# Kernel tuning notes

Hardware: AMD Instinct MI355X
Metric: run time of the kernel (lower is better)

The kernel has to match this reference:

```python
import math
import jax, jax.numpy as jnp
import numpy as np

# Module config (init_kwargs)
GRID = (11, 16, 24)          # (T, H, W) latent grid, T odd so T-1 == 2*(T//2)
POOL = 128                   # pool_size / block size
SPARSITY = 0.9
TXT_LEN = 384                # txt_len, txt_first=False
HEADS, HDIM = 8, 128
FFL = GRID[1] * GRID[2]      # first_frame_len = H*W = 384
SEQ = GRID[0] * FFL + TXT_LEN  # 4608 tokens, 36 blocks of 128


def _rearr(t):
    # rearrange_with_remaining, h%8==0 and w%8==0 path.
    # t: [b, (f h w), n, d] with f = T-1 frames (first frame excluded)
    b, s, n, d = t.shape
    T, H, W = GRID
    fn, hn, wn = T // 2, H // 8, W // 8
    x = t.transpose(0, 2, 1, 3).reshape(b * n, fn, 2, hn, 8, wn, 8, d)
    # 'b (fn fb)(hn hb)(wn wb) d -> b (fn hn wn fb hb wb) d'
    x = x.transpose(0, 1, 3, 5, 2, 4, 6, 7).reshape(b * n, s, d)
    return x.reshape(b, n, s, d).transpose(0, 2, 1, 3)


def _inv_rearr(t):
    b, s, n, d = t.shape
    T, H, W = GRID
    fn, hn, wn = T // 2, H // 8, W // 8
    x = t.transpose(0, 2, 1, 3).reshape(b * n, fn, hn, wn, 2, 8, 8, d)
    x = x.transpose(0, 1, 4, 2, 5, 3, 6, 7).reshape(b * n, s, d)
    return x.reshape(b, n, s, d).transpose(0, 2, 1, 3)


def _avgpool(t):
    # seq divisible by POOL -> mean over each block (tail branch unused)
    b, s, n, d = t.shape
    return t.reshape(b, s // POOL, POOL, n, d).mean(axis=2)


def _forward(q, k, v):
    b, s, n, d = q.shape
    scale = jnp.asarray(d, q.dtype) ** -0.5
    # do_tensor_rearrange_pooling on concatenated qkv (txt_first=False)
    qkv = jnp.concatenate([q, k, v], axis=0)
    f_part = qkv[:, :FFL]
    i_part = qkv[:, FFL:s - TXT_LEN]
    t_part = qkv[:, s - TXT_LEN:]
    qkv2 = jnp.concatenate([_rearr(i_part), f_part, t_part], axis=1)
    pool = _avgpool(qkv2)
    q2, k2, v2 = jnp.split(qkv2, 3, axis=0)
    qp, kp, _ = jnp.split(pool, 3, axis=0)
    # pooled block scores + softmax
    ps = jax.nn.softmax(jnp.einsum('blnd,bsnd->bnls', qp, kp) * scale, axis=-1)
    nb = s // POOL
    keep = math.ceil(nb * (1.0 - SPARSITY))
    thr = jax.lax.top_k(ps, keep)[0][..., -1:]
    mask = ps >= thr                              # [B, n, nb, nb] bool
    prot = (FFL + TXT_LEN + POOL - 1) // POOL
    mask = mask.at[:, :, -prot:, :].set(True)
    mask = mask.at[:, :, :, -prot:].set(True)
    bm = mask[0]                                  # [n, nb, nb] per-head block mask (batch 0, as kernel uses)
    tok = jnp.repeat(jnp.repeat(bm, POOL, axis=1), POOL, axis=2)  # [n, S, S]
    # block-sparse attention == masked dense attention over selected kv blocks
    scores = jnp.einsum('bqnd,bknd->bnqk', q2, k2) * scale
    scores = jnp.where(tok[None], scores, jnp.asarray(-1e30, scores.dtype))
    p = jax.nn.softmax(scores, axis=-1)
    x = jnp.einsum('bnqk,bknd->bqnd', p, v2)
    # do_tensor_inv_rearrange (txt_first=False: concat(f, i, t))
    si = s - TXT_LEN - FFL
    xi = _inv_rearr(x[:, :si])
    xf = x[:, si:si + FFL]
    xt = x[:, si + FFL:]
    return jnp.concatenate([xf, xi, xt], axis=1)


def setup_inputs() -> dict:
    key = jax.random.key(0)
    kq, kk, kv = jax.random.split(key, 3)
    q = jax.random.normal(kq, (1, SEQ, HEADS, HDIM), dtype=jnp.float32)
    k = jax.random.normal(kk, (1, SEQ, HEADS, HDIM), dtype=jnp.float32)
    v = jax.random.normal(kv, (1, SEQ, HEADS, HDIM), dtype=jnp.float32)
    t_b_idx = jnp.arange(2, dtype=jnp.int64 if jax.config.jax_enable_x64 else jnp.int32)
    return {'q': q, 'k': k, 'v': v, 't_b_idx': t_b_idx}


def reference(q, k, v, t_b_idx):
    # t_idx = t_b_idx[0] = 0, skip_timesteps = 0 -> sparse branch (static)
    return _forward(q, k, v)
```

## Files before the change

### kernel.cpp

```cpp
#include <hip/hip_runtime.h>


typedef __attribute__((ext_vector_type(8))) _Float16 half8;
typedef __attribute__((ext_vector_type(4))) _Float16 half4;
typedef __attribute__((ext_vector_type(4))) float float4v;

#define KROW 136
#define VROW 72
#define PROW 72

__device__ __forceinline__ int orig_pos(int j) {
    if (j >= 3840) return (j < 4224) ? (j - 3840) : j;
    int blk = j >> 7;
    int r   = j & 127;
    int f   = blk / 6;
    int rem = blk - f * 6;
    int b2  = rem / 3;
    int e   = rem - b2 * 3;
    int a   = r >> 6;
    int c   = (r >> 3) & 7;
    int g   = r & 7;
    return 384 + (f * 2 + a) * 384 + (b2 * 8 + c) * 24 + e * 8 + g;
}

__device__ __forceinline__ void cp16(const void* g, void* l) {
    __builtin_amdgcn_global_load_lds((const __attribute__((address_space(1))) void*)g,
                                     (__attribute__((address_space(3))) void*)l, 16, 0, 0);
}

__global__ __launch_bounds__(256) void prep_kernel(const float* __restrict__ q,
                                                   const float* __restrict__ k,
                                                   const float* __restrict__ v,
                                                   short* __restrict__ Kc,
                                                   unsigned* __restrict__ Vt32,
                                                   float* __restrict__ qp,
                                                   float* __restrict__ kp) {
    __shared__ short Vs[64 * KROW];
    __shared__ float Rs[8 * 128];
    int bx  = blockIdx.x;
    int tid = threadIdx.x;
    int sub = bx & 1;
    int kb  = (bx >> 1) % 36;
    int h   = bx / 72;

    {
        int lr = tid >> 3;
        int ld = (tid & 7) << 2;
#pragma unroll
        for (int pass = 0; pass < 2; ++pass) {
            int lt  = pass * 32 + lr;
            int tok = sub * 64 + lt;
            int op  = orig_pos(kb * 128 + tok);
            const float* kr = k + ((size_t)op * 8 + h) * 128;
            const float* vr = v + ((size_t)op * 8 + h) * 128;
            short* ko = Kc + ((size_t)(h * 36 + kb) * 128 + tok) * KROW;
#pragma unroll
            for (int j = 0; j < 4; ++j) {
                int d = ld + j * 32;
                float4v xk = *reinterpret_cast<const float4v*>(kr + d);
                float4v xv = *reinterpret_cast<const float4v*>(vr + d);
                half4 hk, hv;
#pragma unroll
                for (int i = 0; i < 4; ++i) { hk[i] = (_Float16)xk[i]; hv[i] = (_Float16)xv[i]; }
                *reinterpret_cast<half4*>(ko + d) = hk;
                *reinterpret_cast<half4*>(&Vs[lt * KROW + d]) = hv;
            }
        }
    }

    {
        const float* arr = sub ? q : k;
        int dq = (tid & 31) << 2;
        int g  = tid >> 5;
        float4v acc = {0.f, 0.f, 0.f, 0.f};
        for (int t = g; t < 128; t += 8) {
            int op = orig_pos(kb * 128 + t);
            float4v x = *reinterpret_cast<const float4v*>(arr + ((size_t)op * 8 + h) * 128 + dq);
            acc[0] += x[0]; acc[1] += x[1]; acc[2] += x[2]; acc[3] += x[3];
        }
#pragma unroll
        for (int i = 0; i < 4; ++i) Rs[g * 128 + dq + i] = acc[i];
    }
    __syncthreads();

    {
        const unsigned short* Vsu = (const unsigned short*)Vs;
        unsigned* vo = Vt32 + (size_t)((h * 36 + kb) * 2 + sub) * 128 * (VROW / 2);
#pragma unroll
        for (int it = 0; it < 16; ++it) {
            int i   = it * 256 + tid;
            int tw  = i & 31;
            int dim = i >> 5;
            unsigned lo = Vsu[(2 * tw) * KROW + dim];
            unsigned hi = Vsu[(2 * tw + 1) * KROW + dim];
            vo[dim * (VROW / 2) + tw] = (hi << 16) | lo;
        }
    }

    if (tid < 128) {
        float s = 0.f;
#pragma unroll
        for (int g = 0; g < 8; ++g) s += Rs[g * 128 + tid];
        float* outp = sub ? qp : kp;
        outp[(h * 36 + kb) * 128 + tid] = s * (1.f / 128.f);
    }
}

__global__ __launch_bounds__(256, 3) void flash_kernel(const float* __restrict__ q,
                                                       const short* __restrict__ Kc,
                                                       const short* __restrict__ Vt,
                                                       const float* __restrict__ qp,
                                                       const float* __restrict__ kp,
                                                       float* __restrict__ out,
                                                       float* __restrict__ pO,
                                                       float* __restrict__ pL) {
    __shared__ __align__(16) short Ks[64 * KROW];
    __shared__ __align__(16) short Vsh[128 * VROW];
    __shared__ __align__(16) short Ph[4 * 16 * PROW];
    __shared__ int Ls[40];

    int t = blockIdx.x;
    int h, qb, half, nkb = 0, kbase = 0, pidx = -1;
    if (t < 288) {
        h = t & 7;
        int rest = t >> 3;
        int qbh = rest / 6, r2 = rest % 6;
        half = r2 / 3;
        int chunk = r2 % 3;
        qb = 30 + qbh; nkb = 12; kbase = chunk * 12; pidx = t;
    } else {
        int t2 = t - 288;
        h = t2 & 7;
        int rest = t2 >> 3;
        qb = rest >> 1; half = rest & 1;
    }

    int tid = threadIdx.x, wave = tid >> 6, lane = tid & 63;
    int m16 = lane & 15, quad = lane >> 4;

    int qrow_frag = qb * 128 + half * 64 + wave * 16 + m16;
    const float* qrp = q + ((size_t)orig_pos(qrow_frag) * 8 + h) * 128;
    half8 aq[4];
#pragma unroll
    for (int kc = 0; kc < 4; ++kc) {
        float4v x0 = *reinterpret_cast<const float4v*>(qrp + kc * 32 + quad * 8);
        float4v x1 = *reinterpret_cast<const float4v*>(qrp + kc * 32 + quad * 8 + 4);
#pragma unroll
        for (int j = 0; j < 4; ++j) { aq[kc][j] = (_Float16)x0[j]; aq[kc][4 + j] = (_Float16)x1[j]; }
    }

    if (pidx < 0 && wave == 0) {
        float s = -1e30f;
        if (lane < 36) {
            const float4v* qv = (const float4v*)(qp + (h * 36 + qb) * 128);
            const float4v* kv = (const float4v*)(kp + (h * 36 + lane) * 128);
            float acc = 0.f;
            for (int i = 0; i < 32; ++i) {
                float4v a = qv[i], b = kv[i];
                acc += a[0] * b[0] + a[1] * b[1] + a[2] * b[2] + a[3] * b[3];
            }
            s = acc;
        }
        float tmp = s;
        float thr = 0.f;
        for (int i = 0; i < 4; ++i) {
            float mx = tmp;
            for (int off = 1; off < 64; off <<= 1) mx = fmaxf(mx, __shfl_xor(mx, off));
            thr = mx;
            unsigned long long bal = __ballot(tmp == mx);
            int low = __ffsll(bal) - 1;
            if (lane == low) tmp = -3e38f;
        }
        bool keep = (lane < 36) && ((s >= thr) || (lane >= 30));
        unsigned long long mk = __ballot(keep);
        if (lane == 0) Ls[0] = __popcll(mk);
        if (keep) {
            int pos = __popcll(mk & ((1ull << lane) - 1ull));
            Ls[1 + pos] = lane;
        }
    }
    __syncthreads();
    if (pidx < 0) nkb = Ls[0];

    float l_r[4], o[8][4];
#pragma unroll
    for (int r = 0; r < 4; ++r) l_r[r] = 0.f;
#pragma unroll
    for (int dt = 0; dt < 8; ++dt)
#pragma unroll
        for (int r = 0; r < 4; ++r) o[dt][r] = 0.f;

    constexpr float kScale = 0.08838834764831845f * 1.4426950408889634f;
    short* Phw = Ph + wave * (16 * PROW);

    int ntile = nkb * 2;
    for (int it = 0; it < ntile; ++it) {
        int kb  = (pidx >= 0) ? (kbase + (it >> 1)) : Ls[1 + (it >> 1)];
        int sub = it & 1;
        const char* gK = (const char*)(Kc + ((size_t)((h * 36 + kb) * 128) + sub * 64) * KROW);
        const char* gV = (const char*)(Vt + (size_t)((h * 36 + kb) * 2 + sub) * 128 * VROW);

        __syncthreads();
        {
            char* lK = (char*)Ks;
            char* lV = (char*)Vsh;
            int off = lane * 16;
            for (int c = wave; c < 35; c += 4) {
                if (c < 17) cp16(gK + c * 1024 + off, lK + c * 1024 + off);
                else        cp16(gV + (c - 17) * 1024 + off, lV + (c - 17) * 1024 + off);
            }
        }
        __syncthreads();

        float4v sacc[4];
#pragma unroll
        for (int nt = 0; nt < 4; ++nt) { sacc[nt][0] = 0.f; sacc[nt][1] = 0.f; sacc[nt][2] = 0.f; sacc[nt][3] = 0.f; }
#pragma unroll
        for (int nt = 0; nt < 4; ++nt)
#pragma unroll
            for (int kc = 0; kc < 4; ++kc) {
                half8 bk = *reinterpret_cast<const half8*>(&Ks[(nt * 16 + m16) * KROW + kc * 32 + quad * 8]);
                sacc[nt] = __builtin_amdgcn_mfma_f32_16x16x32_f16(aq[kc], bk, sacc[nt], 0, 0, 0);
            }

#pragma unroll
        for (int r = 0; r < 4; ++r) {
            float p0 = exp2f(sacc[0][r] * kScale);
            float p1 = exp2f(sacc[1][r] * kScale);
            float p2 = exp2f(sacc[2][r] * kScale);
            float p3 = exp2f(sacc[3][r] * kScale);
            sacc[0][r] = p0; sacc[1][r] = p1; sacc[2][r] = p2; sacc[3][r] = p3;
            l_r[r] += (p0 + p1) + (p2 + p3);
        }

#pragma unroll
        for (int nt = 0; nt < 4; ++nt)
#pragma unroll
            for (int r = 0; r < 4; ++r) {
                union { _Float16 hf; short s; } cv;
                cv.hf = (_Float16)sacc[nt][r];
                Phw[(quad * 4 + r) * PROW + nt * 16 + m16] = cv.s;
            }
        half8 ap0 = *reinterpret_cast<const half8*>(&Phw[m16 * PROW + quad * 8]);
        half8 ap1 = *reinterpret_cast<const half8*>(&Phw[m16 * PROW + 32 + quad * 8]);

#pragma unroll
        for (int dt = 0; dt < 8; ++dt) {
            float4v oc;
            oc[0] = o[dt][0]; oc[1] = o[dt][1]; oc[2] = o[dt][2]; oc[3] = o[dt][3];
            half8 bv0 = *reinterpret_cast<const half8*>(&Vsh[(dt * 16 + m16) * VROW + quad * 8]);
            half8 bv1 = *reinterpret_cast<const half8*>(&Vsh[(dt * 16 + m16) * VROW + 32 + quad * 8]);
            oc = __builtin_amdgcn_mfma_f32_16x16x32_f16(ap0, bv0, oc, 0, 0, 0);
            oc = __builtin_amdgcn_mfma_f32_16x16x32_f16(ap1, bv1, oc, 0, 0, 0);
            o[dt][0] = oc[0]; o[dt][1] = oc[1]; o[dt][2] = oc[2]; o[dt][3] = oc[3];
        }
    }

#pragma unroll
    for (int r = 0; r < 4; ++r)
        for (int sh = 1; sh < 16; sh <<= 1) l_r[r] += __shfl_xor(l_r[r], sh);

    if (pidx >= 0) {
        float* po = pO + (size_t)pidx * 8192;
#pragma unroll
        for (int r = 0; r < 4; ++r) {
            int row = wave * 16 + quad * 4 + r;
#pragma unroll
            for (int dt = 0; dt < 8; ++dt)
                po[row * 128 + dt * 16 + m16] = o[dt][r];
            if (m16 == 0) pL[pidx * 64 + row] = l_r[r];
        }
    } else {
#pragma unroll
        for (int r = 0; r < 4; ++r) {
            int qrow = qb * 128 + half * 64 + wave * 16 + quad * 4 + r;
            size_t base = ((size_t)orig_pos(qrow) * 8 + h) * 128;
            float inv = 1.f / l_r[r];
#pragma unroll
            for (int dt = 0; dt < 8; ++dt)
                out[base + dt * 16 + m16] = o[dt][r] * inv;
        }
    }
}

__global__ void combine_kernel(const float* __restrict__ pO, const float* __restrict__ pL,
                               float* __restrict__ out) {
    int g = blockIdx.x;
    int h    = g / 12;
    int rem  = g % 12;
    int qbh  = rem >> 1;
    int half = rem & 1;
    int qb   = 30 + qbh;
    int base_t = (qbh * 6 + half * 3) * 8 + h;

    int tid = threadIdx.x;
    int d   = tid & 127;
    int r0  = tid >> 7;
    for (int itr = 0; itr < 32; ++itr) {
        int row = r0 + itr * 2;
        float l = pL[(base_t + 0) * 64 + row] + pL[(base_t + 8) * 64 + row] + pL[(base_t + 16) * 64 + row];
        float acc = pO[(size_t)(base_t + 0) * 8192 + row * 128 + d]
                  + pO[(size_t)(base_t + 8) * 8192 + row * 128 + d]
                  + pO[(size_t)(base_t + 16) * 8192 + row * 128 + d];
        int qrow = qb * 128 + half * 64 + row;
        out[((size_t)orig_pos(qrow) * 8 + h) * 128 + d] = acc / l;
    }
}

extern "C" void kernel_launch(void* const* d_in, const int* in_sizes, int n_in,
                              void* d_out, int out_size, void* d_ws, size_t ws_size,
                              hipStream_t stream) {
    const float* q = (const float*)d_in[0];
    const float* k = (const float*)d_in[1];
    const float* v = (const float*)d_in[2];
    float* out = (float*)d_out;

    char* w = (char*)d_ws;
    short* Kc  = (short*)(w);
    short* Vt  = (short*)(w + 10027008);
    float* qp  = (float*)(w + 20643840);
    float* kp  = (float*)(w + 20791296);
    float* pL  = (float*)(w + 20938752);
    float* pO  = (float*)(w + 21012480);

    prep_kernel<<<dim3(576), dim3(256), 0, stream>>>(q, k, v, Kc, (unsigned*)Vt, qp, kp);
    flash_kernel<<<dim3(768), dim3(256), 0, stream>>>(q, Kc, Vt, qp, kp, out, pO, pL);
    combine_kernel<<<dim3(96), dim3(256), 0, stream>>>(pO, pL, out);
}
```

Measured before the change: 191.2 us.

## Use 32x32 MFMA with 128-row query blocks and fuse split-K combine via atomics

Moves the flash kernel from 16x16x32 to 32x32x16 MFMA so each block handles 128 query rows (32 per wave) instead of 64. The heavy protected rows are split four ways over 9 key blocks each rather than three ways over 12. The separate combine kernel is replaced by a last-arriver reduction driven by an atomic counter, and the softmax scale is folded into Q at load time. This cuts the grid to 432 blocks, removes one kernel launch and halves K/V reloads per query row. In exchange it uses more registers (occupancy hint lowered to 2), adds a memset, and needs threadfence and atomic synchronisation.

Result: slower. 217.6 us (+13.8%).

```diff
diff --git a/kernel.cpp b/kernel.cpp
--- a/kernel.cpp
+++ b/kernel.cpp
@@ -4,6 +4,7 @@
 typedef __attribute__((ext_vector_type(8))) _Float16 half8;
 typedef __attribute__((ext_vector_type(4))) _Float16 half4;
 typedef __attribute__((ext_vector_type(4))) float float4v;
+typedef __attribute__((ext_vector_type(16))) float float16v;
 
 #define KROW 136
 #define VROW 72
@@ -26,6 +27,12 @@
 __device__ __forceinline__ void cp16(const void* g, void* l) {
     __builtin_amdgcn_global_load_lds((const __attribute__((address_space(1))) void*)g,
                                      (__attribute__((address_space(3))) void*)l, 16, 0, 0);
+}
+
+__device__ __forceinline__ short h16(float x) {
+    union { _Float16 hf; short s; } cv;
+    cv.hf = (_Float16)x;
+    return cv.s;
 }
 
 __global__ __launch_bounds__(256) void prep_kernel(const float* __restrict__ q,
@@ -106,50 +113,53 @@
     }
 }
 
-__global__ __launch_bounds__(256, 3) void flash_kernel(const float* __restrict__ q,
+__global__ __launch_bounds__(256, 2) void flash_kernel(const float* __restrict__ q,
                                                        const short* __restrict__ Kc,
                                                        const short* __restrict__ Vt,
                                                        const float* __restrict__ qp,
                                                        const float* __restrict__ kp,
                                                        float* __restrict__ out,
                                                        float* __restrict__ pO,
-                                                       float* __restrict__ pL) {
+                                                       float* __restrict__ pL,
+                                                       int* __restrict__ cnt) {
     __shared__ __align__(16) short Ks[64 * KROW];
     __shared__ __align__(16) short Vsh[128 * VROW];
-    __shared__ __align__(16) short Ph[4 * 16 * PROW];
+    __shared__ __align__(16) short Ph[4 * 32 * PROW];
     __shared__ int Ls[40];
 
     int t = blockIdx.x;
-    int h, qb, half, nkb = 0, kbase = 0, pidx = -1;
-    if (t < 288) {
+    int h, qb, qbh = 0, nkb = 0, kbase = 0, task = -1, grp = -1;
+    bool heavy = (t < 192);
+    if (heavy) {
         h = t & 7;
         int rest = t >> 3;
-        int qbh = rest / 6, r2 = rest % 6;
-        half = r2 / 3;
-        int chunk = r2 % 3;
-        qb = 30 + qbh; nkb = 12; kbase = chunk * 12; pidx = t;
+        qbh = rest >> 2;
+        int chunk = rest & 3;
+        qb = 30 + qbh; nkb = 9; kbase = chunk * 9;
+        task = t; grp = qbh * 8 + h;
     } else {
-        int t2 = t - 288;
-        h = t2 & 7;
-        int rest = t2 >> 3;
-        qb = rest >> 1; half = rest & 1;
+        int t2 = t - 192;
+        h = t2 & 7; qb = t2 >> 3;
     }
 
     int tid = threadIdx.x, wave = tid >> 6, lane = tid & 63;
-    int m16 = lane & 15, quad = lane >> 4;
-
-    int qrow_frag = qb * 128 + half * 64 + wave * 16 + m16;
-    const float* qrp = q + ((size_t)orig_pos(qrow_frag) * 8 + h) * 128;
-    half8 aq[4];
-#pragma unroll
-    for (int kc = 0; kc < 4; ++kc) {
-        float4v x0 = *reinterpret_cast<const float4v*>(qrp + kc * 32 + quad * 8);
-        float4v x1 = *reinterpret_cast<const float4v*>(qrp + kc * 32 + quad * 8 + 4);
-#pragma unroll
-        for (int j = 0; j < 4; ++j) { aq[kc][j] = (_Float16)x0[j]; aq[kc][4 + j] = (_Float16)x1[j]; }
-    }
-
-    if (pidx < 0 && wave == 0) {
+    int m32 = lane & 31, half = lane >> 5;
+
+    constexpr float kScale = 0.08838834764831845f * 1.4426950408889634f;
+    const float* qrp = q + ((size_t)orig_pos(qb * 128 + wave * 32 + m32) * 8 + h) * 128 + half * 8;
+    half8 aq[8];
+#pragma unroll
+    for (int kc = 0; kc < 8; ++kc) {
+        float4v x0 = *reinterpret_cast<const float4v*>(qrp + kc * 16);
+        float4v x1 = *reinterpret_cast<const float4v*>(qrp + kc * 16 + 4);
+#pragma unroll
+        for (int j = 0; j < 4; ++j) {
+            aq[kc][j]     = (_Float16)(x0[j] * kScale);
+            aq[kc][4 + j] = (_Float16)(x1[j] * kScale);
+        }
+    }
+
+    if (!heavy && wave == 0) {
         float s = -1e30f;
         if (lane < 36) {
             const float4v* qv = (const float4v*)(qp + (h * 36 + qb) * 128);
@@ -180,22 +190,22 @@
         }
     }
     __syncthreads();
-    if (pidx < 0) nkb = Ls[0];
-
-    float l_r[4], o[8][4];
-#pragma unroll
-    for (int r = 0; r < 4; ++r) l_r[r] = 0.f;
-#pragma unroll
-    for (int dt = 0; dt < 8; ++dt)
-#pragma unroll
-        for (int r = 0; r < 4; ++r) o[dt][r] = 0.f;
-
-    constexpr float kScale = 0.08838834764831845f * 1.4426950408889634f;
-    short* Phw = Ph + wave * (16 * PROW);
+    if (!heavy) nkb = Ls[0];
+
+    float16v oc[4];
+    float l_r[16];
+#pragma unroll
+    for (int dn = 0; dn < 4; ++dn)
+#pragma unroll
+        for (int i = 0; i < 16; ++i) oc[dn][i] = 0.f;
+#pragma unroll
+    for (int r = 0; r < 16; ++r) l_r[r] = 0.f;
+
+    short* Phw = Ph + wave * (32 * PROW);
 
     int ntile = nkb * 2;
     for (int it = 0; it < ntile; ++it) {
-        int kb  = (pidx >= 0) ? (kbase + (it >> 1)) : Ls[1 + (it >> 1)];
+        int kb  = heavy ? (kbase + (it >> 1)) : Ls[1 + (it >> 1)];
         int sub = it & 1;
         const char* gK = (const char*)(Kc + ((size_t)((h * 36 + kb) * 128) + sub * 64) * KROW);
         const char* gV = (const char*)(Vt + (size_t)((h * 36 + kb) * 2 + sub) * 128 * VROW);
@@ -212,98 +222,97 @@
         }
         __syncthreads();
 
-        float4v sacc[4];
-#pragma unroll
-        for (int nt = 0; nt < 4; ++nt) { sacc[nt][0] = 0.f; sacc[nt][1] = 0.f; sacc[nt][2] = 0.f; sacc[nt][3] = 0.f; }
-#pragma unroll
-        for (int nt = 0; nt < 4; ++nt)
-#pragma unroll
-            for (int kc = 0; kc < 4; ++kc) {
-                half8 bk = *reinterpret_cast<const half8*>(&Ks[(nt * 16 + m16) * KROW + kc * 32 + quad * 8]);
-                sacc[nt] = __builtin_amdgcn_mfma_f32_16x16x32_f16(aq[kc], bk, sacc[nt], 0, 0, 0);
-            }
-
-#pragma unroll
-        for (int r = 0; r < 4; ++r) {
-            float p0 = exp2f(sacc[0][r] * kScale);
-            float p1 = exp2f(sacc[1][r] * kScale);
-            float p2 = exp2f(sacc[2][r] * kScale);
-            float p3 = exp2f(sacc[3][r] * kScale);
-            sacc[0][r] = p0; sacc[1][r] = p1; sacc[2][r] = p2; sacc[3][r] = p3;
-            l_r[r] += (p0 + p1) + (p2 + p3);
-        }
-
-#pragma unroll
-        for (int nt = 0; nt < 4; ++nt)
-#pragma unroll
-            for (int r = 0; r < 4; ++r) {
-                union { _Float16 hf; short s; } cv;
-                cv.hf = (_Float16)sacc[nt][r];
-                Phw[(quad * 4 + r) * PROW + nt * 16 + m16] = cv.s;
-            }
-        half8 ap0 = *reinterpret_cast<const half8*>(&Phw[m16 * PROW + quad * 8]);
-        half8 ap1 = *reinterpret_cast<const half8*>(&Phw[m16 * PROW + 32 + quad * 8]);
-
-#pragma unroll
-        for (int dt = 0; dt < 8; ++dt) {
-            float4v oc;
-            oc[0] = o[dt][0]; oc[1] = o[dt][1]; oc[2] = o[dt][2]; oc[3] = o[dt][3];
-            half8 bv0 = *reinterpret_cast<const half8*>(&Vsh[(dt * 16 + m16) * VROW + quad * 8]);
-            half8 bv1 = *reinterpret_cast<const half8*>(&Vsh[(dt * 16 + m16) * VROW + 32 + quad * 8]);
-            oc = __builtin_amdgcn_mfma_f32_16x16x32_f16(ap0, bv0, oc, 0, 0, 0);
-            oc = __builtin_amdgcn_mfma_f32_16x16x32_f16(ap1, bv1, oc, 0, 0, 0);
-            o[dt][0] = oc[0]; o[dt][1] = oc[1]; o[dt][2] = oc[2]; o[dt][3] = oc[3];
-        }
-    }
-
-#pragma unroll
-    for (int r = 0; r < 4; ++r)
-        for (int sh = 1; sh < 16; sh <<= 1) l_r[r] += __shfl_xor(l_r[r], sh);
-
-    if (pidx >= 0) {
-        float* po = pO + (size_t)pidx * 8192;
-#pragma unroll
-        for (int r = 0; r < 4; ++r) {
-            int row = wave * 16 + quad * 4 + r;
-#pragma unroll
-            for (int dt = 0; dt < 8; ++dt)
-                po[row * 128 + dt * 16 + m16] = o[dt][r];
-            if (m16 == 0) pL[pidx * 64 + row] = l_r[r];
+        float16v s0, s1;
+#pragma unroll
+        for (int i = 0; i < 16; ++i) { s0[i] = 0.f; s1[i] = 0.f; }
+#pragma unroll
+        for (int kc = 0; kc < 8; ++kc) {
+            half8 b0 = *reinterpret_cast<const half8*>(&Ks[m32 * KROW + kc * 16 + half * 8]);
+            half8 b1 = *reinterpret_cast<const half8*>(&Ks[(32 + m32) * KROW + kc * 16 + half * 8]);
+            s0 = __builtin_amdgcn_mfma_f32_32x32x16_f16(aq[kc], b0, s0, 0, 0, 0);
+            s1 = __builtin_amdgcn_mfma_f32_32x32x16_f16(aq[kc], b1, s1, 0, 0, 0);
+        }
+
+#pragma unroll
+        for (int r = 0; r < 16; ++r) {
+            int rowl = (r & 3) + 8 * (r >> 2) + 4 * half;
+            float p0 = exp2f(s0[r]);
+            float p1 = exp2f(s1[r]);
+            l_r[r] += p0 + p1;
+            Phw[rowl * PROW + m32]      = h16(p0);
+            Phw[rowl * PROW + 32 + m32] = h16(p1);
+        }
+
+        half8 ap[4];
+#pragma unroll
+        for (int kc2 = 0; kc2 < 4; ++kc2)
+            ap[kc2] = *reinterpret_cast<const half8*>(&Phw[m32 * PROW + kc2 * 16 + half * 8]);
+
+#pragma unroll
+        for (int kc2 = 0; kc2 < 4; ++kc2)
+#pragma unroll
+            for (int dn = 0; dn < 4; ++dn) {
+                half8 bv = *reinterpret_cast<const half8*>(&Vsh[(dn * 32 + m32) * VROW + kc2 * 16 + half * 8]);
+                oc[dn] = __builtin_amdgcn_mfma_f32_32x32x16_f16(ap[kc2], bv, oc[dn], 0, 0, 0);
+            }
+    }
+
+#pragma unroll
+    for (int r = 0; r < 16; ++r)
+        for (int sh = 1; sh < 32; sh <<= 1) l_r[r] += __shfl_xor(l_r[r], sh);
+
+    if (!heavy) {
+#pragma unroll
+        for (int r = 0; r < 16; ++r) {
+            int rowl = (r & 3) + 8 * (r >> 2) + 4 * half;
+            size_t base = ((size_t)orig_pos(qb * 128 + wave * 32 + rowl) * 8 + h) * 128;
+            float inv = 1.f / l_r[r];
+#pragma unroll
+            for (int dn = 0; dn < 4; ++dn)
+                out[base + dn * 32 + m32] = oc[dn][r] * inv;
         }
     } else {
-#pragma unroll
-        for (int r = 0; r < 4; ++r) {
-            int qrow = qb * 128 + half * 64 + wave * 16 + quad * 4 + r;
-            size_t base = ((size_t)orig_pos(qrow) * 8 + h) * 128;
-            float inv = 1.f / l_r[r];
-#pragma unroll
-            for (int dt = 0; dt < 8; ++dt)
-                out[base + dt * 16 + m16] = o[dt][r] * inv;
-        }
-    }
-}
-
-__global__ void combine_kernel(const float* __restrict__ pO, const float* __restrict__ pL,
-                               float* __restrict__ out) {
-    int g = blockIdx.x;
-    int h    = g / 12;
-    int rem  = g % 12;
-    int qbh  = rem >> 1;
-    int half = rem & 1;
-    int qb   = 30 + qbh;
-    int base_t = (qbh * 6 + half * 3) * 8 + h;
-
-    int tid = threadIdx.x;
-    int d   = tid & 127;
-    int r0  = tid >> 7;
-    for (int itr = 0; itr < 32; ++itr) {
-        int row = r0 + itr * 2;
-        float l = pL[(base_t + 0) * 64 + row] + pL[(base_t + 8) * 64 + row] + pL[(base_t + 16) * 64 + row];
-        float acc = pO[(size_t)(base_t + 0) * 8192 + row * 128 + d]
-                  + pO[(size_t)(base_t + 8) * 8192 + row * 128 + d]
-                  + pO[(size_t)(base_t + 16) * 8192 + row * 128 + d];
-        int qrow = qb * 128 + half * 64 + row;
-        out[((size_t)orig_pos(qrow) * 8 + h) * 128 + d] = acc / l;
+        float* po = pO + (size_t)task * 16384;
+#pragma unroll
+        for (int r = 0; r < 16; ++r) {
+            int rowl = (r & 3) + 8 * (r >> 2) + 4 * half;
+            int row  = wave * 32 + rowl;
+#pragma unroll
+            for (int dn = 0; dn < 4; ++dn)
+                po[row * 128 + dn * 32 + m32] = oc[dn][r];
+            if (m32 == 0) pL[task * 128 + row] = l_r[r];
+        }
+        __threadfence();
+        __syncthreads();
+        if (tid == 0) Ls[0] = (atomicAdd(&cnt[grp], 1) == 3) ? 1 : 0;
+        __syncthreads();
+        if (Ls[0]) {
+            __threadfence();
+            int t0 = ((qbh * 4 + 0) << 3) | h;
+            int t1 = ((qbh * 4 + 1) << 3) | h;
+            int t2 = ((qbh * 4 + 2) << 3) | h;
+            int t3 = ((qbh * 4 + 3) << 3) | h;
+            int row = tid >> 1;
+            int d0  = (tid & 1) * 64;
+            float l = pL[t0 * 128 + row] + pL[t1 * 128 + row] + pL[t2 * 128 + row] + pL[t3 * 128 + row];
+            float inv = 1.f / l;
+            float* ob = out + ((size_t)orig_pos(qb * 128 + row) * 8 + h) * 128 + d0;
+            const float* p0 = pO + (size_t)t0 * 16384 + row * 128 + d0;
+            const float* p1 = pO + (size_t)t1 * 16384 + row * 128 + d0;
+            const float* p2 = pO + (size_t)t2 * 16384 + row * 128 + d0;
+            const float* p3 = pO + (size_t)t3 * 16384 + row * 128 + d0;
+#pragma unroll
+            for (int i = 0; i < 16; ++i) {
+                float4v a = *reinterpret_cast<const float4v*>(p0 + i * 4);
+                float4v b = *reinterpret_cast<const float4v*>(p1 + i * 4);
+                float4v c = *reinterpret_cast<const float4v*>(p2 + i * 4);
+                float4v d = *reinterpret_cast<const float4v*>(p3 + i * 4);
+                float4v o;
+#pragma unroll
+                for (int j = 0; j < 4; ++j) o[j] = (a[j] + b[j] + c[j] + d[j]) * inv;
+                *reinterpret_cast<float4v*>(ob + i * 4) = o;
+            }
+        }
     }
 }
 
@@ -321,9 +330,10 @@
     float* qp  = (float*)(w + 20643840);
     float* kp  = (float*)(w + 20791296);
     float* pL  = (float*)(w + 20938752);
-    float* pO  = (float*)(w + 21012480);
-
+    int*   cnt = (int*)  (w + 21037056);
+    float* pO  = (float*)(w + 21037312);
+
+    hipMemsetAsync(cnt, 0, 256, stream);
     prep_kernel<<<dim3(576), dim3(256), 0, stream>>>(q, k, v, Kc, (unsigned*)Vt, qp, kp);
-    flash_kernel<<<dim3(768), dim3(256), 0, stream>>>(q, Kc, Vt, qp, kp, out, pO, pL);
-    combine_kernel<<<dim3(96), dim3(256), 0, stream>>>(pO, pL, out);
-}
+    flash_kernel<<<dim3(432), dim3(256), 0, stream>>>(q, Kc, Vt, qp, kp, out, pO, pL, cnt);
+}
```
